# Kernel optimization log

Measured on AMD Instinct MI355X. Metric: run time of the kernel, lower is better.

Reference implementation:

```python
import jax, jax.numpy as jnp
import numpy as np

B, N, D_IN = 128, 128, 1024
H1, D_OUT = 256, 32
K = 8  # num_clusters


def setup_inputs() -> dict:
    key = jax.random.key(0)
    ks = jax.random.split(key, 3)
    x = jax.random.normal(ks[0], (B, N, D_IN), dtype=jnp.float32)
    W1 = jax.random.normal(ks[1], (D_IN, H1), dtype=jnp.float32) * (1.0 / np.sqrt(D_IN))
    b1 = jnp.zeros((H1,), jnp.float32)
    W2 = jax.random.normal(ks[2], (H1, D_OUT), dtype=jnp.float32) * (1.0 / np.sqrt(H1))
    b2 = jnp.zeros((D_OUT,), jnp.float32)
    return {"x": x, "W1": W1, "b1": b1, "W2": W2, "b2": b2}


def _mlp(x, W1, b1, W2, b2):
    # nn.Sequential(GELU, Linear(1024,256), GELU, Linear(256,32)); torch GELU default = exact erf
    h = jax.nn.gelu(x, approximate=False)
    h = h @ W1 + b1
    h = jax.nn.gelu(h, approximate=False)
    return h @ W2 + b2  # [B, N, 32]


def _ward_labels(feats, k):
    """Greedy ward-linkage agglomerative clustering of feats [n, d] -> int labels [n].
    Ward merge cost d(A,B) = |A||B|/(|A|+|B|) * ||c_A - c_B||^2 (Lance-Williams equiv)."""
    n = feats.shape[0]
    eye = jnp.eye(n, dtype=bool)

    def body(t, state):
        cents, sizes, lab = state
        sq = jnp.sum(cents * cents, axis=-1)
        d2 = jnp.maximum(sq[:, None] + sq[None, :] - 2.0 * (cents @ cents.T), 0.0)
        w = (sizes[:, None] * sizes[None, :]) / (sizes[:, None] + sizes[None, :] + 1e-30)
        active = sizes > 0
        valid = (active[:, None] & active[None, :]) & (~eye)
        Dm = jnp.where(valid, w * d2, jnp.inf)
        idx = jnp.argmin(Dm)
        i, j = idx // n, idx % n
        i2 = jnp.minimum(i, j)
        j2 = jnp.maximum(i, j)
        si, sj = sizes[i2], sizes[j2]
        newc = (cents[i2] * si + cents[j2] * sj) / (si + sj)
        cents = cents.at[i2].set(newc)
        sizes = sizes.at[i2].set(si + sj).at[j2].set(0.0)
        lab = jnp.where(lab == j2, i2, lab)
        return cents, sizes, lab

    init = (feats, jnp.ones((n,), feats.dtype), jnp.arange(n))
    cents, sizes, lab = jax.lax.fori_loop(0, n - k, body, init)
    # relabel surviving representative indices to 0..k-1 (ordered by index)
    rank = jnp.cumsum((sizes > 0).astype(jnp.int32)) - 1
    return rank[lab]


def reference(x, W1, b1, W2, b2):
    feats = _mlp(x, W1, b1, W2, b2)          # [B, N, 32]
    labels = jax.vmap(lambda f: _ward_labels(f, K))(feats)  # [B, N] int32
    return labels
```

## Files before the change

### kernel.cpp

```cpp
#include <hip/hip_runtime.h>
#include <math.h>

#define BB 128
#define NN 128
#define DIN 1024
#define H1 256
#define DOUT 32
#define KCL 8
#define NPTS 128
#define MROWS (BB*NN)
#define CSTR 130
#define RSTR 132
#define HSTR 257
#define DEADKEY 0xFFFFFFFF00000000ull

__device__ __forceinline__ float gelu_exact(float v) {
    return 0.5f * v * (1.0f + erff(v * 0.70710678118654752f));
}

__device__ __forceinline__ unsigned long long mkkey(float v, int r, int j) {
    return ((unsigned long long)__float_as_uint(v) << 32) | (unsigned)((r << 7) | j);
}

__device__ __forceinline__ float readlanef(float v, int lane) {
    return __int_as_float(__builtin_amdgcn_readlane(__float_as_int(v), lane));
}

template<int CTRL, int RMASK>
__device__ __forceinline__ unsigned dpp_umin_step(unsigned v) {
    unsigned t = (unsigned)__builtin_amdgcn_update_dpp((int)v, (int)v, CTRL, RMASK, 0xf, false);
    return t < v ? t : v;
}
__device__ __forceinline__ unsigned wave_umin_bcast(unsigned v) {
    v = dpp_umin_step<0x111, 0xf>(v);
    v = dpp_umin_step<0x112, 0xf>(v);
    v = dpp_umin_step<0x114, 0xf>(v);
    v = dpp_umin_step<0x118, 0xf>(v);
    v = dpp_umin_step<0x142, 0xa>(v);
    v = dpp_umin_step<0x143, 0xc>(v);
    return (unsigned)__builtin_amdgcn_readlane((int)v, 63);
}
__device__ __forceinline__ unsigned half_umin(unsigned v) {
    v = dpp_umin_step<0x111, 0xf>(v);
    v = dpp_umin_step<0x112, 0xf>(v);
    v = dpp_umin_step<0x114, 0xf>(v);
    v = dpp_umin_step<0x118, 0xf>(v);
    v = dpp_umin_step<0x142, 0xa>(v);
    return v;
}

__global__ __launch_bounds__(256) void gelu_kernel(const float* __restrict__ x,
                                                   float* __restrict__ gx, int n4) {
    int i = blockIdx.x * 256 + threadIdx.x;
    const int stride = gridDim.x * 256;
    for (; i < n4; i += stride) {
        float4 v = ((const float4*)x)[i];
        v.x = gelu_exact(v.x);
        v.y = gelu_exact(v.y);
        v.z = gelu_exact(v.z);
        v.w = gelu_exact(v.w);
        ((float4*)gx)[i] = v;
    }
}

template<bool FUSE>
__global__ __launch_bounds__(256) void mlp1_kernel(const float* __restrict__ xin,
                                                   const float* __restrict__ W1,
                                                   const float* __restrict__ b1,
                                                   float* __restrict__ h) {
    __shared__ float As[64][68];
    __shared__ float Bs[64][64];
    const int bn = blockIdx.x;
    const int bm = blockIdx.y;
    const int tid = threadIdx.x;
    const int tx = tid & 15, ty = tid >> 4;

    float acc[4][4] = {{0.f}};

    const int arow = tid >> 2;
    const int kc   = (tid & 3) * 4;
    const int wv   = tid >> 6;
    const int ln   = tid & 63;
    const int bkr  = ln >> 4;
    const int bkc  = (ln & 15) * 4;

    const float* xrow = xin + (size_t)(bm * 64 + arow) * DIN;
    const float* wbase = W1 + bn * 64;

    for (int kt = 0; kt < DIN; kt += 64) {
        float4 a0 = *(const float4*)(xrow + kt + kc);
        float4 a1 = *(const float4*)(xrow + kt + kc + 16);
        float4 a2 = *(const float4*)(xrow + kt + kc + 32);
        float4 a3 = *(const float4*)(xrow + kt + kc + 48);
        __syncthreads();
#pragma unroll
        for (int s = 0; s < 4; ++s) {
            const int kr = wv * 16 + s * 4;
            const float* g = wbase + (size_t)(kt + kr + bkr) * H1 + bkc;
            __builtin_amdgcn_global_load_lds(
                (const __attribute__((address_space(1))) unsigned int*)g,
                (__attribute__((address_space(3))) unsigned int*)&Bs[kr][0], 16, 0, 0);
        }
        if (FUSE) {
            As[kc + 0][arow] = gelu_exact(a0.x);
            As[kc + 1][arow] = gelu_exact(a0.y);
            As[kc + 2][arow] = gelu_exact(a0.z);
            As[kc + 3][arow] = gelu_exact(a0.w);
            As[16 + kc + 0][arow] = gelu_exact(a1.x);
            As[16 + kc + 1][arow] = gelu_exact(a1.y);
            As[16 + kc + 2][arow] = gelu_exact(a1.z);
            As[16 + kc + 3][arow] = gelu_exact(a1.w);
            As[32 + kc + 0][arow] = gelu_exact(a2.x);
            As[32 + kc + 1][arow] = gelu_exact(a2.y);
            As[32 + kc + 2][arow] = gelu_exact(a2.z);
            As[32 + kc + 3][arow] = gelu_exact(a2.w);
            As[48 + kc + 0][arow] = gelu_exact(a3.x);
            As[48 + kc + 1][arow] = gelu_exact(a3.y);
            As[48 + kc + 2][arow] = gelu_exact(a3.z);
            As[48 + kc + 3][arow] = gelu_exact(a3.w);
        } else {
            As[kc + 0][arow] = a0.x;
            As[kc + 1][arow] = a0.y;
            As[kc + 2][arow] = a0.z;
            As[kc + 3][arow] = a0.w;
            As[16 + kc + 0][arow] = a1.x;
            As[16 + kc + 1][arow] = a1.y;
            As[16 + kc + 2][arow] = a1.z;
            As[16 + kc + 3][arow] = a1.w;
            As[32 + kc + 0][arow] = a2.x;
            As[32 + kc + 1][arow] = a2.y;
            As[32 + kc + 2][arow] = a2.z;
            As[32 + kc + 3][arow] = a2.w;
            As[48 + kc + 0][arow] = a3.x;
            As[48 + kc + 1][arow] = a3.y;
            As[48 + kc + 2][arow] = a3.z;
            As[48 + kc + 3][arow] = a3.w;
        }
        __syncthreads();
#pragma unroll
        for (int kk = 0; kk < 64; ++kk) {
            float4 a = *(const float4*)&As[kk][ty * 4];
            float4 b = *(const float4*)&Bs[kk][tx * 4];
            float ar[4] = {a.x, a.y, a.z, a.w};
            float br[4] = {b.x, b.y, b.z, b.w};
#pragma unroll
            for (int i = 0; i < 4; ++i)
#pragma unroll
                for (int j = 0; j < 4; ++j)
                    acc[i][j] = fmaf(ar[i], br[j], acc[i][j]);
        }
    }

    const int row = bm * 64 + ty * 4;
    const int col = bn * 64 + tx * 4;
    float4 bias = *(const float4*)(b1 + col);
#pragma unroll
    for (int i = 0; i < 4; ++i) {
        float4 o;
        o.x = acc[i][0] + bias.x;
        o.y = acc[i][1] + bias.y;
        o.z = acc[i][2] + bias.z;
        o.w = acc[i][3] + bias.w;
        *(float4*)(h + (size_t)(row + i) * H1 + col) = o;
    }
}

__global__ __launch_bounds__(256) void mlp2_kernel(const float* __restrict__ h,
                                                   const float* __restrict__ W2,
                                                   const float* __restrict__ b2,
                                                   float* __restrict__ feats) {
    __shared__ float hs[32 * HSTR];
    __shared__ float w2s[H1 * DOUT];
    const int blk = blockIdx.x;
    const int tid = threadIdx.x;

    for (int i = tid; i < (H1 * DOUT) / 4; i += 256)
        ((float4*)w2s)[i] = ((const float4*)W2)[i];

    const float* hb = h + (size_t)blk * 32 * H1;
    const int sr = tid & 31;
    const int sk = (tid >> 5) * 32;
    const float* hrow = hb + (size_t)sr * H1 + sk;
#pragma unroll
    for (int j = 0; j < 8; ++j) {
        float4 v = ((const float4*)hrow)[j];
        hs[sr * HSTR + sk + 4 * j + 0] = gelu_exact(v.x);
        hs[sr * HSTR + sk + 4 * j + 1] = gelu_exact(v.y);
        hs[sr * HSTR + sk + 4 * j + 2] = gelu_exact(v.z);
        hs[sr * HSTR + sk + 4 * j + 3] = gelu_exact(v.w);
    }
    __syncthreads();

    const int row = tid >> 3;
    const int col4 = (tid & 7) * 4;
    const float4 bias = ((const float4*)b2)[tid & 7];
    float a0 = 0.f, a1 = 0.f, a2 = 0.f, a3 = 0.f;
    const float* hr = &hs[row * HSTR];
    for (int k = 0; k < H1; ++k) {
        float a = hr[k];
        float4 w = *(const float4*)&w2s[k * DOUT + col4];
        a0 = fmaf(a, w.x, a0);
        a1 = fmaf(a, w.y, a1);
        a2 = fmaf(a, w.z, a2);
        a3 = fmaf(a, w.w, a3);
    }
    float4 o;
    o.x = a0 + bias.x;
    o.y = a1 + bias.y;
    o.z = a2 + bias.z;
    o.w = a3 + bias.w;
    *(float4*)(feats + (size_t)(blk * 32 + row) * DOUT + col4) = o;
}

__global__ __launch_bounds__(256) void ward_kernel(const float* __restrict__ feats,
                                                   int* __restrict__ out) {
    __shared__ __align__(16) float cost[NPTS * RSTR];
    __shared__ __align__(16) float G[NPTS * RSTR];
    __shared__ float centsT[32 * CSTR];
    __shared__ unsigned long long rowkey[NPTS];
    __shared__ float sqArr[NPTS];
    __shared__ float szsE[NPTS];
    __shared__ int rnk[NPTS];

    const int b = blockIdx.x;
    const int tid = threadIdx.x;
    const float* f = feats + (size_t)b * NPTS * DOUT;
    const float INF = __builtin_inff();

    for (int i = tid; i < NPTS * DOUT; i += 256) {
        int r = i >> 5, d = i & 31;
        centsT[d * CSTR + r] = f[i];
    }
    __syncthreads();
    if (tid < NPTS) {
        float s = 0.f;
#pragma unroll
        for (int d = 0; d < 32; ++d) {
            float v = centsT[d * CSTR + tid];
            s = fmaf(v, v, s);
        }
        sqArr[tid] = s;
    }
    __syncthreads();
    {
        int ti = tid >> 4, tj = tid & 15;
        int I0 = ti * 8, J0 = tj * 8;
        float acc[8][8];
#pragma unroll
        for (int u = 0; u < 8; ++u)
#pragma unroll
            for (int v = 0; v < 8; ++v) acc[u][v] = 0.f;
        for (int d = 0; d < 32; ++d) {
            float a[8], bb[8];
#pragma unroll
            for (int u = 0; u < 8; ++u) a[u] = centsT[d * CSTR + I0 + u];
#pragma unroll
            for (int v = 0; v < 8; ++v) bb[v] = centsT[d * CSTR + J0 + v];
#pragma unroll
            for (int u = 0; u < 8; ++u)
#pragma unroll
                for (int v = 0; v < 8; ++v)
                    acc[u][v] = fmaf(a[u], bb[v], acc[u][v]);
        }
#pragma unroll
        for (int u = 0; u < 8; ++u) {
            const int i = I0 + u;
            const int rq = 4 * ((i >> 1) & 31);
#pragma unroll
            for (int v = 0; v < 8; ++v) {
                int j = J0 + v;
                int pc = (j + rq) & 127;
                G[i * RSTR + pc] = acc[u][v];
                float d2 = sqArr[i] + sqArr[j] - 2.0f * acc[u][v];
                if (d2 < 0.f) d2 = 0.f;
                float w = (1.0f * 1.0f) / (1.0f + 1.0f + 1e-30f);
                cost[i * RSTR + pc] = (i == j) ? INF : w * d2;
            }
        }
    }
    __syncthreads();
    if (tid < NPTS) {
        unsigned long long best = DEADKEY;
        const int rq = 4 * ((tid >> 1) & 31);
        for (int j = 0; j < NPTS; ++j) {
            float v = cost[tid * RSTR + ((j + rq) & 127)];
            unsigned long long k = mkkey(v, tid, j);
            if (k < best) best = k;
        }
        rowkey[tid] = best;
    }
    __syncthreads();

    if (tid >= 64) return;
    const int lane = tid;
    const int hh = lane & 31;
    const int r0 = lane * 2, r1 = lane * 2 + 1;
    const int hq4 = 4 * hh;

    unsigned long long k0 = rowkey[r0], k1 = rowkey[r1];
    float q0 = sqArr[r0], q1 = sqArr[r1];
    float s0 = 1.0f, s1 = 1.0f;
    int lab0 = r0, lab1 = r1;
    unsigned long long alive0 = ~0ull, alive1 = ~0ull;

    for (int it = 0; it < NPTS - KCL; ++it) {
        unsigned bv0 = (unsigned)(k0 >> 32), bv1 = (unsigned)(k1 >> 32);
        unsigned lmin = bv0 < bv1 ? bv0 : bv1;
        unsigned lflat = (bv0 <= bv1) ? (unsigned)(k0 & 0x3FFFu) : (unsigned)(k1 & 0x3FFFu);
        unsigned gmin = wave_umin_bcast(lmin);
        unsigned long long bmask = __ballot(lmin == gmin);
        int lsel = __ffsll(bmask) - 1;
        unsigned flat = (unsigned)__builtin_amdgcn_readlane((int)lflat, lsel);
        int ra = (int)(flat >> 7), ca = (int)(flat & 127u);
        const int i2 = ra < ca ? ra : ca;
        const int j2 = ra < ca ? ca : ra;
        const int ri2 = 4 * ((i2 >> 1) & 31);
        const int rj2 = 4 * ((j2 >> 1) & 31);

        float2 gi = *(const float2*)&G[i2 * RSTR + ((r0 + ri2) & 127)];
        float2 gj = *(const float2*)&G[j2 * RSTR + ((r0 + rj2) & 127)];

        float si = readlanef((i2 & 1) ? s1 : s0, i2 >> 1);
        float sj = readlanef((j2 & 1) ? s1 : s0, j2 >> 1);
        const float snew = si + sj;
        const float invs = 1.0f / snew;
        const float wa = si * invs, wb = sj * invs;

        int arg0 = (int)(k0 & 127u), arg1 = (int)(k1 & 127u);
        bool d0 = (s0 > 0.f) && r0 != i2 && r0 != j2 && (arg0 == i2 || arg0 == j2);
        bool d1 = (s1 > 0.f) && r1 != i2 && r1 != j2 && (arg1 == i2 || arg1 == j2);
        unsigned long long m0 = __ballot(d0), m1 = __ballot(d1);

        float Gii = readlanef((i2 & 1) ? gi.y : gi.x, i2 >> 1);
        float Gij = readlanef((i2 & 1) ? gj.y : gj.x, i2 >> 1);
        float Gjj = readlanef((j2 & 1) ? gj.y : gj.x, j2 >> 1);
        float dotA = wa * Gii + wb * Gij;
        float dotB = wa * Gij + wb * Gjj;
        float qn = wa * dotA + wb * dotB;

        float dot0 = wa * gi.x + wb * gj.x;
        float dot1 = wa * gi.y + wb * gj.y;

        if (lab0 == j2) lab0 = i2;
        if (lab1 == j2) lab1 = i2;
        if (r0 == i2) s0 = snew; else if (r0 == j2) { s0 = 0.f; k0 = DEADKEY; }
        if (r1 == i2) s1 = snew; else if (r1 == j2) { s1 = 0.f; k1 = DEADKEY; }
        if (j2 < 64) alive0 &= ~(1ull << j2); else alive1 &= ~(1ull << (j2 - 64));
        if (r0 == i2) { dot0 = qn; q0 = qn; }
        if (r1 == i2) { dot1 = qn; q1 = qn; }

        *(float2*)&G[i2 * RSTR + ((r0 + ri2) & 127)] = make_float2(dot0, dot1);
        G[r0 * RSTR + ((i2 + hq4) & 127)] = dot0;
        G[r1 * RSTR + ((i2 + hq4) & 127)] = dot1;

        bool w0 = (s0 > 0.f) && r0 != i2 && r0 != j2;
        bool w1 = (s1 > 0.f) && r1 != i2 && r1 != j2;
        if (w0) {
            float d2 = q0 + qn - 2.0f * dot0;
            if (d2 < 0.f) d2 = 0.f;
            float w = (s0 * snew) / (s0 + snew + 1e-30f);
            float v0 = w * d2;
            cost[r0 * RSTR + ((i2 + hq4) & 127)] = v0;
            cost[i2 * RSTR + ((r0 + ri2) & 127)] = v0;
            if (!d0) {
                unsigned long long nk = mkkey(v0, r0, i2);
                if (nk < k0) k0 = nk;
            }
        }
        if (w1) {
            float d2 = q1 + qn - 2.0f * dot1;
            if (d2 < 0.f) d2 = 0.f;
            float w = (s1 * snew) / (s1 + snew + 1e-30f);
            float v1 = w * d2;
            cost[r1 * RSTR + ((i2 + hq4) & 127)] = v1;
            cost[i2 * RSTR + ((r1 + ri2) & 127)] = v1;
            if (!d1) {
                unsigned long long nk = mkkey(v1, r1, i2);
                if (nk < k1) k1 = nk;
            }
        }

        bool pi = true;
        unsigned long long mm0 = m0, mm1 = m1;
        while (pi | (mm0 != 0ull) | (mm1 != 0ull)) {
            int rA, rB;
            bool hasB = false;
            if (pi) { rA = i2; pi = false; }
            else if (mm0) { int t = __ffsll(mm0) - 1; rA = 2 * t; mm0 &= mm0 - 1; }
            else { int t = __ffsll(mm1) - 1; rA = 2 * t + 1; mm1 &= mm1 - 1; }
            if (mm0) { int t = __ffsll(mm0) - 1; rB = 2 * t; mm0 &= mm0 - 1; hasB = true; }
            else if (mm1) { int t = __ffsll(mm1) - 1; rB = 2 * t + 1; mm1 &= mm1 - 1; hasB = true; }
            else rB = rA;

            int r = (lane < 32) ? rA : rB;
            float4 cv = *(const float4*)&cost[r * RSTR + 4 * hh];
            int lq = (hh - ((r >> 1) & 31)) & 31;
            unsigned long long word = (lq < 16) ? alive0 : alive1;
            unsigned nib = (unsigned)(word >> ((4 * lq) & 63)) & 0xFu;
            unsigned e0 = (nib & 1u) ? __float_as_uint(cv.x) : 0xFFFFFFFFu;
            unsigned e1 = (nib & 2u) ? __float_as_uint(cv.y) : 0xFFFFFFFFu;
            unsigned e2 = (nib & 4u) ? __float_as_uint(cv.z) : 0xFFFFFFFFu;
            unsigned e3 = (nib & 8u) ? __float_as_uint(cv.w) : 0xFFFFFFFFu;
            unsigned m = e0; int c = 0;
            if (e1 < m) { m = e1; c = 1; }
            if (e2 < m) { m = e2; c = 2; }
            if (e3 < m) { m = e3; c = 3; }
            int lcol = 4 * lq + c;
            unsigned hm = half_umin(m);
            unsigned vA = (unsigned)__builtin_amdgcn_readlane((int)hm, 31);
            unsigned vB = (unsigned)__builtin_amdgcn_readlane((int)hm, 63);
            unsigned vref = (lane < 32) ? vA : vB;
            unsigned long long msk = __ballot(m == vref);
            int laneA = __ffsll(msk & 0xFFFFFFFFull) - 1;
            int laneB = 32 + __ffsll(msk >> 32) - 1;
            int colA = __builtin_amdgcn_readlane(lcol, laneA);
            int colB = __builtin_amdgcn_readlane(lcol, laneB);
            unsigned long long keyA = ((unsigned long long)vA << 32) | (unsigned)((rA << 7) | colA);
            unsigned long long keyB = ((unsigned long long)vB << 32) | (unsigned)((rB << 7) | colB);
            if (lane == (rA >> 1)) { if (rA & 1) k1 = keyA; else k0 = keyA; }
            if (hasB && lane == (rB >> 1)) { if (rB & 1) k1 = keyB; else k0 = keyB; }
        }
    }

    szsE[r0] = s0;
    szsE[r1] = s1;
    __asm__ volatile("s_waitcnt lgkmcnt(0)" ::: "memory");
    if (lane == 0) {
        int c = 0;
        for (int i = 0; i < NPTS; ++i) rnk[i] = (szsE[i] > 0.f) ? c++ : -1;
    }
    __asm__ volatile("s_waitcnt lgkmcnt(0)" ::: "memory");
    out[b * NPTS + r0] = rnk[lab0];
    out[b * NPTS + r1] = rnk[lab1];
}

extern "C" void kernel_launch(void* const* d_in, const int* in_sizes, int n_in,
                              void* d_out, int out_size, void* d_ws, size_t ws_size,
                              hipStream_t stream) {
    const float* x  = (const float*)d_in[0];
    const float* W1 = (const float*)d_in[1];
    const float* b1 = (const float*)d_in[2];
    const float* W2 = (const float*)d_in[3];
    const float* b2 = (const float*)d_in[4];

    float* h = (float*)d_ws;
    float* feats = h + (size_t)MROWS * H1;
    float* gx = feats + (size_t)MROWS * DOUT;
    int* out = (int*)d_out;

    const size_t need = ((size_t)MROWS * H1 + (size_t)MROWS * DOUT + (size_t)MROWS * DIN) * 4;
    const bool use_gx = ws_size >= need;

    if (use_gx) {
        gelu_kernel<<<2048, 256, 0, stream>>>(x, gx, MROWS * DIN / 4);
        mlp1_kernel<false><<<dim3(H1 / 64, MROWS / 64), 256, 0, stream>>>(gx, W1, b1, h);
    } else {
        mlp1_kernel<true><<<dim3(H1 / 64, MROWS / 64), 256, 0, stream>>>(x, W1, b1, h);
    }
    mlp2_kernel<<<MROWS / 32, 256, 0, stream>>>(h, W2, b2, feats);
    ward_kernel<<<BB, 256, 0, stream>>>(feats, out);
}
```

Baseline: 446.1 us.

## Use Lance-Williams Ward update on cost matrix instead of Gram matrix

Replaces the per-merge Gram-matrix update (dot products and norms of merged centroids) with the Lance-Williams recurrence applied directly to the Ward cost matrix. This drops the G shared array, freeing about 66KB of LDS, and removes the rotated column swizzle on cost. Each merge needs fewer LDS reads, writes and cross-lane reads. The trade-off is that the recurrence accumulates rounding differently from recomputing distances, which could change tie-breaking or merge order, and the unswizzled layout may bring back LDS bank conflicts on the column writes.

```diff
diff --git a/kernel.cpp b/kernel.cpp
--- a/kernel.cpp
+++ b/kernel.cpp
@@ -215,7 +215,6 @@
 __global__ __launch_bounds__(256) void ward_kernel(const float* __restrict__ feats,
                                                    int* __restrict__ out) {
     __shared__ __align__(16) float cost[NPTS * RSTR];
-    __shared__ __align__(16) float G[NPTS * RSTR];
     __shared__ float centsT[32 * CSTR];
     __shared__ unsigned long long rowkey[NPTS];
     __shared__ float sqArr[NPTS];
@@ -264,26 +263,21 @@
         }
 #pragma unroll
         for (int u = 0; u < 8; ++u) {
-            const int i = I0 + u;
-            const int rq = 4 * ((i >> 1) & 31);
 #pragma unroll
             for (int v = 0; v < 8; ++v) {
-                int j = J0 + v;
-                int pc = (j + rq) & 127;
-                G[i * RSTR + pc] = acc[u][v];
+                int i = I0 + u, j = J0 + v;
                 float d2 = sqArr[i] + sqArr[j] - 2.0f * acc[u][v];
                 if (d2 < 0.f) d2 = 0.f;
                 float w = (1.0f * 1.0f) / (1.0f + 1.0f + 1e-30f);
-                cost[i * RSTR + pc] = (i == j) ? INF : w * d2;
+                cost[i * RSTR + j] = (i == j) ? INF : w * d2;
             }
         }
     }
     __syncthreads();
     if (tid < NPTS) {
         unsigned long long best = DEADKEY;
-        const int rq = 4 * ((tid >> 1) & 31);
         for (int j = 0; j < NPTS; ++j) {
-            float v = cost[tid * RSTR + ((j + rq) & 127)];
+            float v = cost[tid * RSTR + j];
             unsigned long long k = mkkey(v, tid, j);
             if (k < best) best = k;
         }
@@ -295,10 +289,8 @@
     const int lane = tid;
     const int hh = lane & 31;
     const int r0 = lane * 2, r1 = lane * 2 + 1;
-    const int hq4 = 4 * hh;
 
     unsigned long long k0 = rowkey[r0], k1 = rowkey[r1];
-    float q0 = sqArr[r0], q1 = sqArr[r1];
     float s0 = 1.0f, s1 = 1.0f;
     int lab0 = r0, lab1 = r1;
     unsigned long long alive0 = ~0ull, alive1 = ~0ull;
@@ -314,68 +306,46 @@
         int ra = (int)(flat >> 7), ca = (int)(flat & 127u);
         const int i2 = ra < ca ? ra : ca;
         const int j2 = ra < ca ? ca : ra;
-        const int ri2 = 4 * ((i2 >> 1) & 31);
-        const int rj2 = 4 * ((j2 >> 1) & 31);
-
-        float2 gi = *(const float2*)&G[i2 * RSTR + ((r0 + ri2) & 127)];
-        float2 gj = *(const float2*)&G[j2 * RSTR + ((r0 + rj2) & 127)];
+        const float Dij = __uint_as_float(gmin);
+
+        float2 ci = *(const float2*)&cost[i2 * RSTR + r0];
+        float2 cj = *(const float2*)&cost[j2 * RSTR + r0];
 
         float si = readlanef((i2 & 1) ? s1 : s0, i2 >> 1);
         float sj = readlanef((j2 & 1) ? s1 : s0, j2 >> 1);
         const float snew = si + sj;
-        const float invs = 1.0f / snew;
-        const float wa = si * invs, wb = sj * invs;
 
         int arg0 = (int)(k0 & 127u), arg1 = (int)(k1 & 127u);
         bool d0 = (s0 > 0.f) && r0 != i2 && r0 != j2 && (arg0 == i2 || arg0 == j2);
         bool d1 = (s1 > 0.f) && r1 != i2 && r1 != j2 && (arg1 == i2 || arg1 == j2);
         unsigned long long m0 = __ballot(d0), m1 = __ballot(d1);
 
-        float Gii = readlanef((i2 & 1) ? gi.y : gi.x, i2 >> 1);
-        float Gij = readlanef((i2 & 1) ? gj.y : gj.x, i2 >> 1);
-        float Gjj = readlanef((j2 & 1) ? gj.y : gj.x, j2 >> 1);
-        float dotA = wa * Gii + wb * Gij;
-        float dotB = wa * Gij + wb * Gjj;
-        float qn = wa * dotA + wb * dotB;
-
-        float dot0 = wa * gi.x + wb * gj.x;
-        float dot1 = wa * gi.y + wb * gj.y;
+        float Dn0 = ((si + s0) * ci.x + (sj + s0) * cj.x - s0 * Dij) / (snew + s0);
+        float Dn1 = ((si + s1) * ci.y + (sj + s1) * cj.y - s1 * Dij) / (snew + s1);
+        if (Dn0 < 0.f) Dn0 = 0.f;
+        if (Dn1 < 0.f) Dn1 = 0.f;
 
         if (lab0 == j2) lab0 = i2;
         if (lab1 == j2) lab1 = i2;
         if (r0 == i2) s0 = snew; else if (r0 == j2) { s0 = 0.f; k0 = DEADKEY; }
         if (r1 == i2) s1 = snew; else if (r1 == j2) { s1 = 0.f; k1 = DEADKEY; }
         if (j2 < 64) alive0 &= ~(1ull << j2); else alive1 &= ~(1ull << (j2 - 64));
-        if (r0 == i2) { dot0 = qn; q0 = qn; }
-        if (r1 == i2) { dot1 = qn; q1 = qn; }
-
-        *(float2*)&G[i2 * RSTR + ((r0 + ri2) & 127)] = make_float2(dot0, dot1);
-        G[r0 * RSTR + ((i2 + hq4) & 127)] = dot0;
-        G[r1 * RSTR + ((i2 + hq4) & 127)] = dot1;
 
         bool w0 = (s0 > 0.f) && r0 != i2 && r0 != j2;
         bool w1 = (s1 > 0.f) && r1 != i2 && r1 != j2;
         if (w0) {
-            float d2 = q0 + qn - 2.0f * dot0;
-            if (d2 < 0.f) d2 = 0.f;
-            float w = (s0 * snew) / (s0 + snew + 1e-30f);
-            float v0 = w * d2;
-            cost[r0 * RSTR + ((i2 + hq4) & 127)] = v0;
-            cost[i2 * RSTR + ((r0 + ri2) & 127)] = v0;
+            cost[r0 * RSTR + i2] = Dn0;
+            cost[i2 * RSTR + r0] = Dn0;
             if (!d0) {
-                unsigned long long nk = mkkey(v0, r0, i2);
+                unsigned long long nk = mkkey(Dn0, r0, i2);
                 if (nk < k0) k0 = nk;
             }
         }
         if (w1) {
-            float d2 = q1 + qn - 2.0f * dot1;
-            if (d2 < 0.f) d2 = 0.f;
-            float w = (s1 * snew) / (s1 + snew + 1e-30f);
-            float v1 = w * d2;
-            cost[r1 * RSTR + ((i2 + hq4) & 127)] = v1;
-            cost[i2 * RSTR + ((r1 + ri2) & 127)] = v1;
+            cost[r1 * RSTR + i2] = Dn1;
+            cost[i2 * RSTR + r1] = Dn1;
             if (!d1) {
-                unsigned long long nk = mkkey(v1, r1, i2);
+                unsigned long long nk = mkkey(Dn1, r1, i2);
                 if (nk < k1) k1 = nk;
             }
         }
@@ -394,9 +364,8 @@
 
             int r = (lane < 32) ? rA : rB;
             float4 cv = *(const float4*)&cost[r * RSTR + 4 * hh];
-            int lq = (hh - ((r >> 1) & 31)) & 31;
-            unsigned long long word = (lq < 16) ? alive0 : alive1;
-            unsigned nib = (unsigned)(word >> ((4 * lq) & 63)) & 0xFu;
+            unsigned long long word = (hh < 16) ? alive0 : alive1;
+            unsigned nib = (unsigned)(word >> ((4 * hh) & 63)) & 0xFu;
             unsigned e0 = (nib & 1u) ? __float_as_uint(cv.x) : 0xFFFFFFFFu;
             unsigned e1 = (nib & 2u) ? __float_as_uint(cv.y) : 0xFFFFFFFFu;
             unsigned e2 = (nib & 4u) ? __float_as_uint(cv.z) : 0xFFFFFFFFu;
@@ -405,7 +374,7 @@
             if (e1 < m) { m = e1; c = 1; }
             if (e2 < m) { m = e2; c = 2; }
             if (e3 < m) { m = e3; c = 3; }
-            int lcol = 4 * lq + c;
+            int lcol = 4 * hh + c;
             unsigned hm = half_umin(m);
             unsigned vA = (unsigned)__builtin_amdgcn_readlane((int)hm, 31);
             unsigned vB = (unsigned)__builtin_amdgcn_readlane((int)hm, 63);
```

Result: faster. 431.9 us (-3.2%).
